# Performance work log

Measured on AMD Instinct MI355X. Metric: run time of the kernel, lower is better.

Reference implementation:

```python
import jax, jax.numpy as jnp
import numpy as np
from jax import lax

D_MODEL = 256; D_HEAD = 32; NHEAD = 8; WIN = 8; TOPK = 8; DMID = 1024
B = 2; H = 128; WD = 128
BN_EPS = 1e-5; ATT_EPS = 1e-6

def _bn(x, g, b, m, v):
    # inference-mode BatchNorm2d over NCHW
    s = g / jnp.sqrt(v + BN_EPS)
    return x * s[None, :, None, None] + (b - m * s)[None, :, None, None]

def _gelu(x):
    return jax.nn.gelu(x, approximate=False)  # torch nn.GELU default (erf)

def _conv1x1(x, w, bias=None):
    y = jnp.einsum('bchw,oc->bohw', x, w)
    if bias is not None:
        y = y + bias[None, :, None, None]
    return y

def _to_win(t):
    b, d, h, wd = t.shape
    nh, nw = h // WIN, wd // WIN
    t = t.reshape(b, d, nh, WIN, nw, WIN).transpose(0, 2, 4, 3, 5, 1)
    return t.reshape(b, nh * nw, WIN * WIN, d)

def _from_win(m, h, wd):
    b, n, w2, d = m.shape
    nh, nw = h // WIN, wd // WIN
    m = m.reshape(b, nh, nw, WIN, WIN, d).transpose(0, 5, 1, 3, 2, 4)
    return m.reshape(b, d, h, wd)

def _linear_attention(q, k, v):
    # LoFTR linear attention. q: [n, L, H, D]; k, v: [n, S, H, D]
    Q = jax.nn.elu(q) + 1.0
    K = jax.nn.elu(k) + 1.0
    s_len = v.shape[1]
    vals = v / s_len
    KV = jnp.einsum('nshd,nshv->nhdv', K, vals)
    Z = 1.0 / (jnp.einsum('nlhd,nhd->nlh', Q, K.sum(axis=1)) + ATT_EPS)
    return jnp.einsum('nlhd,nhdv,nlh->nlhv', Q, KV, Z) * s_len

def _topk_window_attention(q, k, v):
    # partition into WINxWIN windows, select top-K key windows per query window
    # by mean-pooled window similarity, gather them, attend within each window.
    b, d, h, wd = q.shape
    qw, kw, vw = _to_win(q), _to_win(k), _to_win(v)  # [b, N, W2, d]
    n = qw.shape[1]; w2 = WIN * WIN
    sim = jnp.einsum('bnd,bmd->bnm', qw.mean(axis=2), kw.mean(axis=2))
    idx = lax.top_k(sim, TOPK)[1]  # [b, N, K]
    gather = jax.vmap(lambda t, i: t[i])  # over batch: [N,W2,d],[N,K] -> [N,K,W2,d]
    kg = gather(kw, idx).reshape(b, n, TOPK * w2, d)
    vg = gather(vw, idx).reshape(b, n, TOPK * w2, d)
    Q = qw.reshape(b * n, w2, NHEAD, D_HEAD)
    K = kg.reshape(b * n, TOPK * w2, NHEAD, D_HEAD)
    V = vg.reshape(b * n, TOPK * w2, NHEAD, D_HEAD)
    out = _linear_attention(Q, K, V).reshape(b, n, w2, d)
    return _from_win(out, h, wd)

def _forward(x0, bn0_g, bn0_b, bn0_m, bn0_v, q_w, k_w, v_w, merge_w, merge_b,
             mlp_w1, bn1_g, bn1_b, bn1_m, bn1_v, mlp_dw,
             bn2_g, bn2_b, bn2_m, bn2_v, mlp_w2, bn3_g, bn3_b, bn3_m, bn3_v):
    _x = _gelu(_bn(x0, bn0_g, bn0_b, bn0_m, bn0_v))  # pre_normact (x1 = x0)
    q = _conv1x1(_x, q_w); k = _conv1x1(_x, k_w); v = _conv1x1(_x, v_w)
    msg = _topk_window_attention(q, k, v)
    x = x0 + _conv1x1(msg, merge_w, merge_b)  # merge + residual (DropPath=id)
    # MB mlp block: 1x1 -> BN -> GELU -> dw3x3 -> BN -> GELU -> 1x1 -> BN
    y = _conv1x1(x, mlp_w1)
    y = _gelu(_bn(y, bn1_g, bn1_b, bn1_m, bn1_v))
    y = lax.conv_general_dilated(y, mlp_dw, (1, 1), 'SAME',
                                 feature_group_count=DMID,
                                 dimension_numbers=('NCHW', 'OIHW', 'NCHW'))
    y = _gelu(_bn(y, bn2_g, bn2_b, bn2_m, bn2_v))
    y = _conv1x1(y, mlp_w2)
    y = _bn(y, bn3_g, bn3_b, bn3_m, bn3_v)
    return x + y

def setup_inputs() -> dict:
    ks = jax.random.split(jax.random.key(0), 26)
    nrm = lambda i, shape, s=1.0: jax.random.normal(ks[i], shape, jnp.float32) * s
    uni = lambda i, shape: jax.random.uniform(ks[i], shape, jnp.float32, 0.5, 1.5)
    sc = float(1.0 / np.sqrt(D_MODEL))
    return {
        'x0': nrm(0, (B, D_MODEL, H, WD)),
        'bn0_g': uni(1, (D_MODEL,)), 'bn0_b': nrm(2, (D_MODEL,), 0.1),
        'bn0_m': nrm(3, (D_MODEL,), 0.1), 'bn0_v': uni(4, (D_MODEL,)),
        'q_w': nrm(5, (D_MODEL, D_MODEL), sc),
        'k_w': nrm(6, (D_MODEL, D_MODEL), sc),
        'v_w': nrm(7, (D_MODEL, D_MODEL), sc),
        'merge_w': nrm(8, (D_MODEL, D_MODEL), sc), 'merge_b': nrm(9, (D_MODEL,), 0.1),
        'mlp_w1': nrm(10, (DMID, D_MODEL), sc),
        'bn1_g': uni(11, (DMID,)), 'bn1_b': nrm(12, (DMID,), 0.1),
        'bn1_m': nrm(13, (DMID,), 0.1), 'bn1_v': uni(14, (DMID,)),
        'mlp_dw': nrm(15, (DMID, 1, 3, 3), 1.0 / 3.0),
        'bn2_g': uni(16, (DMID,)), 'bn2_b': nrm(17, (DMID,), 0.1),
        'bn2_m': nrm(18, (DMID,), 0.1), 'bn2_v': uni(19, (DMID,)),
        'mlp_w2': nrm(20, (D_MODEL, DMID), float(1.0 / np.sqrt(DMID))),
        'bn3_g': uni(21, (D_MODEL,)), 'bn3_b': nrm(22, (D_MODEL,), 0.1),
        'bn3_m': nrm(23, (D_MODEL,), 0.1), 'bn3_v': uni(24, (D_MODEL,)),
    }

def reference(x0, bn0_g, bn0_b, bn0_m, bn0_v, q_w, k_w, v_w, merge_w, merge_b,
              mlp_w1, bn1_g, bn1_b, bn1_m, bn1_v, mlp_dw,
              bn2_g, bn2_b, bn2_m, bn2_v, mlp_w2, bn3_g, bn3_b, bn3_m, bn3_v):
    return _forward(x0, bn0_g, bn0_b, bn0_m, bn0_v, q_w, k_w, v_w, merge_w, merge_b,
                    mlp_w1, bn1_g, bn1_b, bn1_m, bn1_v, mlp_dw,
                    bn2_g, bn2_b, bn2_m, bn2_v, mlp_w2, bn3_g, bn3_b, bn3_m, bn3_v)
```

## Files before the change

kernel.cpp:

```cpp
#include <hip/hip_runtime.h>
#include <hip/hip_bf16.h>
#include <type_traits>

typedef __hip_bfloat16 bf16;
typedef __attribute__((ext_vector_type(8))) short s16x8;
typedef __attribute__((ext_vector_type(4))) short s16x4;
typedef __attribute__((ext_vector_type(4))) float f32x4;

#define DEVI __device__ __forceinline__

DEVI float bf2f(bf16 x) { return __bfloat162float(x); }
DEVI float to_f(float x) { return x; }
DEVI float to_f(bf16 x) { return __bfloat162float(x); }
DEVI float gelu_f(float x) {
  const float y = x * 0.7071067811865476f;
  const float a = fabsf(y);
  const float t = __builtin_amdgcn_rcpf(1.0f + 0.3275911f * a);
  const float p = t * (0.254829592f + t * (-0.284496736f +
                  t * (1.421413741f + t * (-1.453152027f + t * 1.061405429f))));
  const float e = __expf(-a * a);
  const float erfv = copysignf(1.0f - p * e, y);
  return 0.5f * x * (1.0f + erfv);
}
DEVI float elu1(float x) { return x > 0.f ? x + 1.f : __expf(x); }
DEVI float s2f(short s) {
  unsigned u = ((unsigned)(unsigned short)s) << 16;
  float f; __builtin_memcpy(&f, &u, 4); return f;
}
DEVI short f2s(float x) {
  bf16 h = __float2bfloat16(x);
  short s; __builtin_memcpy(&s, &h, 2); return s;
}

__global__ void detect_kernel(const void* x0, int* dflag) {
  const int t = threadIdx.x;
  const bf16* p = (const bf16*)x0;
  float v = bf2f(p[t * 2]);
  bool ok = (fabsf(v) <= 64.0f);
  unsigned long long m = __ballot(ok);
  if (t == 0) dflag[0] = (m == ~0ull) ? 0 : 1;
}

template <typename TIN>
__global__ __launch_bounds__(256) void bnprep_kernel(
    const int* dflag, int want,
    const TIN* g0, const TIN* b0, const TIN* m0, const TIN* v0,
    const TIN* g1, const TIN* b1, const TIN* m1, const TIN* v1,
    const TIN* g2, const TIN* b2, const TIN* m2, const TIN* v2,
    const TIN* g3, const TIN* b3, const TIN* m3, const TIN* v3,
    const TIN* mb, float* out)
{
  if (dflag[0] != want) return;
  int t = threadIdx.x;
  {
    float s = to_f(g0[t]) / sqrtf(to_f(v0[t]) + 1e-5f);
    out[t] = s; out[256 + t] = to_f(b0[t]) - to_f(m0[t]) * s;
  }
  for (int i = t; i < 1024; i += 256) {
    float s = to_f(g1[i]) / sqrtf(to_f(v1[i]) + 1e-5f);
    out[512 + i] = s; out[1536 + i] = to_f(b1[i]) - to_f(m1[i]) * s;
  }
  for (int i = t; i < 1024; i += 256) {
    float s = to_f(g2[i]) / sqrtf(to_f(v2[i]) + 1e-5f);
    out[2560 + i] = s; out[3584 + i] = to_f(b2[i]) - to_f(m2[i]) * s;
  }
  {
    float s = to_f(g3[t]) / sqrtf(to_f(v3[t]) + 1e-5f);
    out[4608 + t] = s; out[4864 + t] = to_f(b3[t]) - to_f(m3[t]) * s;
    out[5120 + t] = to_f(mb[t]);
  }
}

template <typename TIN>
__global__ __launch_bounds__(256) void wconv_kernel(
    const int* dflag, int want,
    const TIN* qw, const TIN* kw, const TIN* vw, const TIN* mw,
    const TIN* w1, const TIN* w2, const TIN* dw, bf16* dst)
{
  if (dflag[0] != want) return;
  int i = blockIdx.x * 256 + threadIdx.x;
  if (i >= 795648) return;
  const TIN* src; int off;
  if (i < 262144) {
    src = (i < 65536) ? qw : (i < 131072) ? kw : (i < 196608) ? vw : mw;
    off = i & 65535;
  } else if (i < 524288) { src = w1; off = i - 262144; }
  else if (i < 786432) { src = w2; off = i - 524288; }
  else {
    src = dw;
    const int o = i - 786432;
    const int tap = o >> 10, m = o & 1023;
    off = m * 9 + tap;
    if (o >= 9216) return;
  }
  dst[i] = __float2bfloat16(to_f(src[off]));
}

template <typename TIN>
__global__ __launch_bounds__(256) void prenorm_t_kernel(
    const int* dflag, int want, const TIN* __restrict__ x0,
    const float* __restrict__ bn, bf16* __restrict__ xhat_t)
{
  if (dflag[0] != want) return;
  __shared__ float T[128][67];
  const int t = threadIdx.x;
  const int tile = blockIdx.x;
  const int b = tile >> 8;
  const int p0 = (tile & 255) * 64;
  const long xbase = (long)b * 4194304 + p0;
  const int px_off = (t & 7) * 8;
  const int chr = t >> 3;
  const int ch8 = (t & 15) * 8;
  const int pxw = t >> 4;
  #pragma unroll
  for (int pass = 0; pass < 2; ++pass) {
    const int Hc = pass * 128;
    __syncthreads();
    #pragma unroll
    for (int cc = 0; cc < 4; ++cc) {
      const int ch = Hc + chr + 32 * cc;
      const TIN* xp = x0 + (long)ch * 16384 + xbase + px_off;
      float v[8];
      if constexpr (sizeof(TIN) == 2) {
        const s16x8 r = *(const s16x8*)xp;
        #pragma unroll
        for (int j = 0; j < 8; ++j) v[j] = s2f(r[j]);
      } else {
        const float4 a = *(const float4*)xp;
        const float4 c = *(const float4*)(xp + 4);
        v[0] = a.x; v[1] = a.y; v[2] = a.z; v[3] = a.w;
        v[4] = c.x; v[5] = c.y; v[6] = c.z; v[7] = c.w;
      }
      const float s0 = bn[ch], t0 = bn[256 + ch];
      #pragma unroll
      for (int j = 0; j < 8; ++j) v[j] = gelu_f(v[j] * s0 + t0);
      float* Tr = &T[chr + 32 * cc][px_off];
      #pragma unroll
      for (int j = 0; j < 8; ++j) Tr[j] = v[j];
    }
    __syncthreads();
    #pragma unroll
    for (int it = 0; it < 4; ++it) {
      const int px = pxw + 16 * it;
      alignas(16) short o[8];
      #pragma unroll
      for (int j = 0; j < 8; ++j) o[j] = f2s(T[ch8 + j][px]);
      *(uint4*)(xhat_t + (long)(b * 16384 + p0 + px) * 256 + Hc + ch8) =
          *(const uint4*)o;
    }
  }
}

template <int MODE, typename TRES = bf16>
__global__ __launch_bounds__(256) void mfma_gemm(
    const int* dflag, int want,
    const bf16* __restrict__ in, const bf16* __restrict__ w,
    void* __restrict__ out, long obase, const void* __restrict__ resv,
    const float* __restrict__ sv, const float* __restrict__ tv,
    float* __restrict__ aux, int N, int M, int K)
{
  if (want >= 0 && dflag[0] != want) return;
  alignas(16) __shared__ char smem[(MODE <= 2) ? 20480 : 34816];
  bf16* inT = (bf16*)smem;
  bf16* wT  = (bf16*)(smem + 10240);
  const int t = threadIdx.x;
  const int n0 = blockIdx.x * 128, m0 = blockIdx.y * 128;
  const int sr = t >> 1, sk = (t & 1) * 16;
  const int wid = t >> 6, lane = t & 63;
  const int nw = (wid & 1) * 64, mw = (wid >> 1) * 64;
  const int l15 = lane & 15, quad = lane >> 4;
  f32x4 acc[4][4];
  #pragma unroll
  for (int i = 0; i < 4; ++i)
    #pragma unroll
    for (int j = 0; j < 4; ++j) acc[i][j] = 0.f;
  long inRow;
  if (MODE == 4) {
    const int bb4 = n0 >> 14, w0 = (n0 & 16383) >> 6;
    const int win = w0 + (sr >> 6);
    const int rr = (sr >> 3) & 7, cc = sr & 7;
    inRow = ((long)(bb4 * 16384 + ((win >> 4) * 8 + rr) * 128
                    + (win & 15) * 8 + cc)) * K + sk;
  } else {
    inRow = (long)(n0 + sr) * K + sk;
  }
  const long wRow = (long)(m0 + sr) * K + sk;
  for (int k0 = 0; k0 < K; k0 += 32) {
    const uint4 a0 = *(const uint4*)(in + inRow + k0);
    const uint4 a1 = *(const uint4*)(in + inRow + k0 + 8);
    const uint4 b0 = *(const uint4*)(w + wRow + k0);
    const uint4 b1 = *(const uint4*)(w + wRow + k0 + 8);
    __syncthreads();
    *(uint4*)(inT + sr * 40 + sk) = a0;
    *(uint4*)(inT + sr * 40 + sk + 8) = a1;
    *(uint4*)(wT + sr * 40 + sk) = b0;
    *(uint4*)(wT + sr * 40 + sk + 8) = b1;
    __syncthreads();
    s16x8 af[4], bfv[4];
    #pragma unroll
    for (int i = 0; i < 4; ++i)
      af[i] = *(const s16x8*)(inT + (nw + i * 16 + l15) * 40 + quad * 8);
    #pragma unroll
    for (int i = 0; i < 4; ++i)
      bfv[i] = *(const s16x8*)(wT + (mw + i * 16 + l15) * 40 + quad * 8);
    #pragma unroll
    for (int i = 0; i < 4; ++i)
      #pragma unroll
      for (int j = 0; j < 4; ++j)
        acc[i][j] = __builtin_amdgcn_mfma_f32_16x16x32_bf16(af[i], bfv[j], acc[i][j], 0, 0, 0);
  }
  if (MODE <= 2) {
    bf16* ob = (bf16*)out;
    const bool doelu = (MODE == 0) && (m0 < 512);
    #pragma unroll
    for (int i = 0; i < 4; ++i) {
      #pragma unroll
      for (int r = 0; r < 4; ++r) {
        const int n = n0 + nw + i * 16 + quad * 4 + r;
        #pragma unroll
        for (int j = 0; j < 4; ++j) {
          const int m = m0 + mw + j * 16 + l15;
          float vv = acc[i][j][r];
          if (MODE == 0) { if (doelu) vv = elu1(vv); }
          if (MODE == 1) {
            const TRES* res = (const TRES*)resv;
            vv += sv[m] + to_f(res[(long)(n >> 14) * 4194304
                                   + (long)m * 16384 + (n & 16383)]);
          }
          if (MODE == 2) vv = gelu_f(vv * sv[m] + tv[m]);
          ob[(long)n * M + m] = __float2bfloat16(vv);
        }
      }
    }
  } else {
    const int isf = (MODE == 3) ? dflag[0] : 0;
    __syncthreads();
    bf16* T = (bf16*)smem;
    #pragma unroll
    for (int i = 0; i < 4; ++i)
      #pragma unroll
      for (int r = 0; r < 4; ++r) {
        const int n = nw + i * 16 + quad * 4 + r;
        #pragma unroll
        for (int j = 0; j < 4; ++j) {
          const int m = mw + j * 16 + l15;
          float vv = acc[i][j][r];
          if (MODE == 3)
            vv = vv * sv[m0 + m] + tv[m0 + m]
               + bf2f(((const bf16*)resv)[(long)(n0 + n) * 256 + m0 + m]);
          else { if (m0 + m < 256) vv = elu1(vv); }
          T[m * 136 + n] = __float2bfloat16(vv);
        }
      }
    __syncthreads();
    const int mr = t >> 1, half = (t & 1) * 64;
    if (MODE == 4) {
      const int bb4 = n0 >> 14, w0 = (n0 & 16383) >> 6;
      const int gm = m0 + mr;
      bf16* bo = (bf16*)out;
      #pragma unroll
      for (int jj = 0; jj < 8; ++jj) {
        const int C = half + jj * 8;
        const int win = w0 + (C >> 6);
        const int pxc = (C & 63) >> 3;
        *(uint4*)(bo + ((long)(bb4 * 256 + win) << 15) + pxc * 4096 + gm * 8) =
            *(const uint4*)(T + mr * 136 + C);
      }
      if (m0 < 256) {
        float s = 0.f;
        const bf16* Tr = T + mr * 136 + half;
        #pragma unroll
        for (int c8 = 0; c8 < 8; ++c8) {
          const s16x8 v = *(const s16x8*)(Tr + c8 * 8);
          #pragma unroll
          for (int e = 0; e < 8; ++e) s += s2f(v[e]);
        }
        aux[(long)(bb4 * 256 + w0 + (half >> 6)) * 256 + gm] = s;
      }
    } else if (!isf) {
      bf16* bo = (bf16*)out + obase;
      #pragma unroll
      for (int jj = 0; jj < 8; ++jj)
        *(uint4*)(bo + (long)(m0 + mr) * N + n0 + half + jj * 8) =
            *(const uint4*)(T + mr * 136 + half + jj * 8);
    } else {
      float* fo = (float*)out + obase;
      #pragma unroll
      for (int jj = 0; jj < 8; ++jj)
        #pragma unroll
        for (int e = 0; e < 8; ++e)
          fo[(long)(m0 + mr) * N + n0 + half + jj * 8 + e] =
              bf2f(T[mr * 136 + half + jj * 8 + e]);
    }
  }
}

template <typename TIN>
__global__ __launch_bounds__(256) void xmean_kernel(const int* dflag, int want,
                                                    const TIN* __restrict__ x0,
                                                    const float* __restrict__ bn,
                                                    float* __restrict__ xm)
{
  if (dflag[0] != want) return;
  int tid = blockIdx.x * 256 + threadIdx.x;
  int n = tid & 255, c = (tid >> 8) & 255, b = tid >> 16;
  const float s0 = bn[c], t0 = bn[256 + c];
  const long base = (long)b * 4194304 + (long)c * 16384 + ((n >> 4) * 8) * 128 + (n & 15) * 8;
  float s = 0.f;
  #pragma unroll
  for (int r = 0; r < 8; ++r)
    #pragma unroll
    for (int cc = 0; cc < 8; ++cc)
      s += gelu_f(to_f(x0[base + r * 128 + cc]) * s0 + t0);
  xm[tid] = s * 0.015625f;
}

template <typename TIN>
__global__ __launch_bounds__(256) void meanproj_kernel(const int* dflag, int want,
    const TIN* __restrict__ qw, const TIN* __restrict__ kw,
    const float* __restrict__ xm, float* __restrict__ qm, float* __restrict__ km)
{
  if (dflag[0] != want) return;
  int tid = blockIdx.x * 256 + threadIdx.x;
  int nw = tid & 255, o = (tid >> 8) & 255, b = tid >> 16;
  float sq = 0.f, sk = 0.f;
  for (int c = 0; c < 256; ++c) {
    const float x = xm[(b * 256 + c) * 256 + nw];
    sq += to_f(qw[o * 256 + c]) * x;
    sk += to_f(kw[o * 256 + c]) * x;
  }
  qm[(b * 256 + o) * 256 + nw] = sq;
  km[(b * 256 + o) * 256 + nw] = sk;
}

__global__ __launch_bounds__(256) void topk_kernel(const float* __restrict__ qm,
                                                   const float* __restrict__ km,
                                                   int* __restrict__ topki)
{
  const int nq = blockIdx.x, b = blockIdx.y, t = threadIdx.x;
  float sim = 0.f;
  for (int c = 0; c < 256; ++c)
    sim += qm[(b * 256 + c) * 256 + nq] * km[(b * 256 + c) * 256 + t];
  __shared__ float vals[256];
  __shared__ float rv[256];
  __shared__ int ri[256];
  vals[t] = sim;
  __syncthreads();
  for (int j = 0; j < 8; ++j) {
    rv[t] = vals[t]; ri[t] = t;
    __syncthreads();
    for (int off = 128; off > 0; off >>= 1) {
      if (t < off) {
        float v2 = rv[t + off]; int i2 = ri[t + off];
        if (v2 > rv[t] || (v2 == rv[t] && i2 < ri[t])) { rv[t] = v2; ri[t] = i2; }
      }
      __syncthreads();
    }
    const int w = ri[0];
    if (t == 0) topki[(b * 256 + nq) * 8 + j] = w;
    __syncthreads();
    if (t == w) vals[t] = -3.0e38f;
    __syncthreads();
  }
}

__global__ __launch_bounds__(256) void attn_kernel(
    const bf16* __restrict__ qbuf, const bf16* __restrict__ kvT,
    const int* __restrict__ topki, const float* __restrict__ S,
    bf16* __restrict__ msg)
{
  __shared__ bf16 kvB[10240];
  __shared__ float ksum_s[256];
  __shared__ float zs2[512];
  const int n = blockIdx.x, b = blockIdx.y, t = threadIdx.x;
  const long bpix = (long)b * 16384;
  const int lane = t & 63, wid = t >> 6;
  const int l15 = lane & 15, quad = lane >> 4;
  const int h0 = wid * 2;
  f32x4 kvacc[2][2][2];
  #pragma unroll
  for (int a = 0; a < 2; ++a)
    #pragma unroll
    for (int c = 0; c < 2; ++c)
      #pragma unroll
      for (int d = 0; d < 2; ++d) kvacc[a][c][d] = 0.f;
  int wsel[8];
  #pragma unroll
  for (int j = 0; j < 8; ++j) wsel[j] = topki[(b * 256 + n) * 8 + j];

  const long kvTb = (long)b * 8388608;
  #pragma unroll 8
  for (int ck = 0; ck < 16; ++ck) {
    const bf16* base = kvT + kvTb + ((long)wsel[ck >> 1] << 15)
                     + ((ck & 1) * 4 + quad) * 4096;
    #pragma unroll
    for (int hs = 0; hs < 2; ++hs) {
      const int cb = (h0 + hs) * 32;
      const s16x8 a0 = *(const s16x8*)(base + (cb + l15) * 8);
      const s16x8 a1 = *(const s16x8*)(base + (cb + 16 + l15) * 8);
      const s16x8 b0 = *(const s16x8*)(base + (256 + cb + l15) * 8);
      const s16x8 b1 = *(const s16x8*)(base + (256 + cb + 16 + l15) * 8);
      kvacc[hs][0][0] = __builtin_amdgcn_mfma_f32_16x16x32_bf16(a0, b0, kvacc[hs][0][0], 0, 0, 0);
      kvacc[hs][0][1] = __builtin_amdgcn_mfma_f32_16x16x32_bf16(a0, b1, kvacc[hs][0][1], 0, 0, 0);
      kvacc[hs][1][0] = __builtin_amdgcn_mfma_f32_16x16x32_bf16(a1, b0, kvacc[hs][1][0], 0, 0, 0);
      kvacc[hs][1][1] = __builtin_amdgcn_mfma_f32_16x16x32_bf16(a1, b1, kvacc[hs][1][1], 0, 0, 0);
    }
  }

  {
    float ks = 0.f;
    #pragma unroll
    for (int j = 0; j < 8; ++j)
      ks += S[((long)b * 256 + wsel[j]) * 256 + t];
    ksum_s[t] = ks;
  }
  #pragma unroll
  for (int hs = 0; hs < 2; ++hs)
    #pragma unroll
    for (int vt = 0; vt < 2; ++vt) {
      const int row = (h0 + hs) * 32 + vt * 16 + l15;
      #pragma unroll
      for (int dt = 0; dt < 2; ++dt) {
        const f32x4 kv = kvacc[hs][dt][vt];
        uint2 u;
        u.x = (unsigned)(unsigned short)f2s(kv[0])
            | ((unsigned)(unsigned short)f2s(kv[1]) << 16);
        u.y = (unsigned)(unsigned short)f2s(kv[2])
            | ((unsigned)(unsigned short)f2s(kv[3]) << 16);
        *(uint2*)(kvB + row * 40 + dt * 16 + quad * 4) = u;
      }
    }
  __syncthreads();

  const int qh0 = (n >> 4) * 8, qw0 = (n & 15) * 8;
  #pragma unroll
  for (int rep = 0; rep < 2; ++rep) {
    const int idx = t + rep * 256;
    const int l = idx >> 3, hh = idx & 7;
    const long gp = bpix + (qh0 + (l >> 3)) * 128 + qw0 + (l & 7);
    const bf16* qp = qbuf + gp * 256 + hh * 32;
    float dot = 0.f;
    #pragma unroll
    for (int k4 = 0; k4 < 4; ++k4) {
      const s16x8 q8 = *(const s16x8*)(qp + k4 * 8);
      const float4 kA = *(const float4*)(ksum_s + hh * 32 + k4 * 8);
      const float4 kB = *(const float4*)(ksum_s + hh * 32 + k4 * 8 + 4);
      dot += s2f(q8[0]) * kA.x + s2f(q8[1]) * kA.y
           + s2f(q8[2]) * kA.z + s2f(q8[3]) * kA.w
           + s2f(q8[4]) * kB.x + s2f(q8[5]) * kB.y
           + s2f(q8[6]) * kB.z + s2f(q8[7]) * kB.w;
    }
    zs2[hh * 64 + l] = 1.f / (dot + 1e-6f);
  }
  __syncthreads();

  #pragma unroll
  for (int hs = 0; hs < 2; ++hs) {
    const int h = h0 + hs;
    const s16x8 B0 = *(const s16x8*)(kvB + (h * 32 + l15) * 40 + quad * 8);
    const s16x8 B1 = *(const s16x8*)(kvB + (h * 32 + 16 + l15) * 40 + quad * 8);
    #pragma unroll
    for (int i = 0; i < 4; ++i) {
      const int lq = i * 16 + l15;
      const long gpa = bpix + (qh0 + (lq >> 3)) * 128 + qw0 + (lq & 7);
      const s16x8 A = *(const s16x8*)(qbuf + gpa * 256 + h * 32 + quad * 8);
      f32x4 o0 = 0.f, o1 = 0.f;
      o0 = __builtin_amdgcn_mfma_f32_16x16x32_bf16(A, B0, o0, 0, 0, 0);
      o1 = __builtin_amdgcn_mfma_f32_16x16x32_bf16(A, B1, o1, 0, 0, 0);
      const float4 z4 = *(const float4*)(zs2 + h * 64 + i * 16 + quad * 4);
      const float zr[4] = {z4.x, z4.y, z4.z, z4.w};
      #pragma unroll
      for (int r = 0; r < 4; ++r) {
        const int lo = i * 16 + quad * 4 + r;
        const long opix = bpix + (qh0 + (lo >> 3)) * 128 + qw0 + (lo & 7);
        msg[opix * 256 + h * 32 + l15] = __float2bfloat16(o0[r] * zr[r]);
        msg[opix * 256 + h * 32 + 16 + l15] = __float2bfloat16(o1[r] * zr[r]);
      }
    }
  }
}

__global__ __launch_bounds__(256) void dwconv_kernel(const bf16* __restrict__ y1,
                                                     const bf16* __restrict__ wdw,
                                                     const float* __restrict__ s2,
                                                     const float* __restrict__ t2,
                                                     bf16* __restrict__ y2)
{
  const int strip = blockIdx.x;
  const int x0 = (strip & 15) * 8;
  const int yy = strip >> 4;
  const int m0 = threadIdx.x * 4;
  float wv[9][4];
  #pragma unroll
  for (int tap = 0; tap < 9; ++tap) {
    const s16x4 w4 = *(const s16x4*)(wdw + tap * 1024 + m0);
    #pragma unroll
    for (int e = 0; e < 4; ++e) wv[tap][e] = s2f(w4[e]);
  }
  float acc[8][4];
  #pragma unroll
  for (int p = 0; p < 8; ++p)
    #pragma unroll
    for (int e = 0; e < 4; ++e) acc[p][e] = 0.f;
  #pragma unroll
  for (int ky = 0; ky < 3; ++ky) {
    const int row = yy + ky - 1;
    if ((unsigned)row < 128u) {
      const bf16* rp = y1 + (long)row * 131072 + m0;
      #pragma unroll
      for (int cr = 0; cr < 10; ++cr) {
        const int xc = x0 + cr - 1;
        if ((unsigned)xc < 128u) {
          const s16x4 v4 = *(const s16x4*)(rp + (long)xc * 1024);
          float vf[4];
          #pragma unroll
          for (int e = 0; e < 4; ++e) vf[e] = s2f(v4[e]);
          #pragma unroll
          for (int kx = 0; kx < 3; ++kx) {
            const int p = cr - kx;
            if (p >= 0 && p < 8) {
              #pragma unroll
              for (int e = 0; e < 4; ++e)
                acc[p][e] += wv[ky * 3 + kx][e] * vf[e];
            }
          }
        }
      }
    }
  }
  const float4 sv = *(const float4*)(s2 + m0);
  const float4 tv = *(const float4*)(t2 + m0);
  #pragma unroll
  for (int p = 0; p < 8; ++p) {
    s16x4 o;
    o[0] = f2s(gelu_f(acc[p][0] * sv.x + tv.x));
    o[1] = f2s(gelu_f(acc[p][1] * sv.y + tv.y));
    o[2] = f2s(gelu_f(acc[p][2] * sv.z + tv.z));
    o[3] = f2s(gelu_f(acc[p][3] * sv.w + tv.w));
    *(s16x4*)(y2 + (long)(yy * 128 + x0 + p) * 1024 + m0) = o;
  }
}

template <typename TIN>
static void stage_dtype_pre(int want, void* const* d_in, hipStream_t stream,
                            const int* dflag, bf16* wb, float* bnbuf,
                            bf16* xhat_t, float* xmean, float* qm, float* km)
{
  bnprep_kernel<TIN><<<1, 256, 0, stream>>>(dflag, want,
      (const TIN*)d_in[1],  (const TIN*)d_in[2],  (const TIN*)d_in[3],  (const TIN*)d_in[4],
      (const TIN*)d_in[11], (const TIN*)d_in[12], (const TIN*)d_in[13], (const TIN*)d_in[14],
      (const TIN*)d_in[16], (const TIN*)d_in[17], (const TIN*)d_in[18], (const TIN*)d_in[19],
      (const TIN*)d_in[21], (const TIN*)d_in[22], (const TIN*)d_in[23], (const TIN*)d_in[24],
      (const TIN*)d_in[9], bnbuf);
  wconv_kernel<TIN><<<3108, 256, 0, stream>>>(dflag, want,
      (const TIN*)d_in[5], (const TIN*)d_in[6], (const TIN*)d_in[7], (const TIN*)d_in[8],
      (const TIN*)d_in[10], (const TIN*)d_in[20], (const TIN*)d_in[15], wb);
  prenorm_t_kernel<TIN><<<512, 256, 0, stream>>>(dflag, want,
      (const TIN*)d_in[0], bnbuf, xhat_t);
  xmean_kernel<TIN><<<512, 256, 0, stream>>>(dflag, want, (const TIN*)d_in[0], bnbuf, xmean);
  meanproj_kernel<TIN><<<512, 256, 0, stream>>>(dflag, want,
      (const TIN*)d_in[5], (const TIN*)d_in[6], xmean, qm, km);
}

extern "C" void kernel_launch(void* const* d_in, const int* in_sizes, int n_in,
                              void* d_out, int out_size, void* d_ws, size_t ws_size,
                              hipStream_t stream) {
  (void)n_in; (void)out_size; (void)ws_size;
  char* W = (char*)d_ws;
  bf16*  xhat_t = (bf16*)(W);
  bf16*  xres   = (bf16*)(W);
  float* Swin   = (float*)(W + 16777216);
  bf16*  qbuf   = (bf16*)(W + 33554432);
  bf16*  kvT    = (bf16*)(W + 50331648);
  bf16*  msg    = (bf16*)(W + 83886080);
  bf16*  y1     = (bf16*)(W + 33554432);
  bf16*  y2     = (bf16*)(W + 67108864);
  char*  S      = W + 100663296;
  bf16*  wb     = (bf16*)(S);
  bf16*  wmb    = wb + 196608;
  bf16*  w1b    = wb + 262144;
  bf16*  w2b    = wb + 524288;
  bf16*  wdwb   = wb + 786432;
  float* bnbuf  = (float*)(S + 1591296);
  float* xmean  = (float*)(S + 1612800);
  float* qm     = (float*)(S + 2137088);
  float* km     = (float*)(S + 2661376);
  int*   topki  = (int*)(S + 3185664);
  int*   dflag  = (int*)(S + 3202048);

  int known = -1;
  if (in_sizes) {
    if (in_sizes[0] == 16777216) known = 0;
    else if (in_sizes[0] == 33554432) known = 1;
  }

  detect_kernel<<<1, 64, 0, stream>>>(d_in[0], dflag);

  if (known != 1)
    stage_dtype_pre<bf16>(0, d_in, stream, dflag, wb, bnbuf, xhat_t, xmean, qm, km);
  if (known != 0)
    stage_dtype_pre<float>(1, d_in, stream, dflag, wb, bnbuf, xhat_t, xmean, qm, km);

  mfma_gemm<0><<<dim3(256, 2), 256, 0, stream>>>(dflag, -1,
      xhat_t, wb, (void*)qbuf, 0, nullptr, nullptr, nullptr, nullptr, 32768, 256, 256);
  mfma_gemm<4><<<dim3(256, 4), 256, 0, stream>>>(dflag, -1,
      xhat_t, wb + 65536, (void*)kvT, 0, nullptr, nullptr, nullptr, Swin, 32768, 512, 256);

  topk_kernel<<<dim3(256, 2), 256, 0, stream>>>(qm, km, topki);
  attn_kernel<<<dim3(256, 2), 256, 0, stream>>>(qbuf, kvT, topki, Swin, msg);

  if (known != 1)
    mfma_gemm<1, bf16><<<dim3(256, 2), 256, 0, stream>>>(dflag, 0,
        msg, wmb, (void*)xres, 0, d_in[0], bnbuf + 5120, nullptr, nullptr, 32768, 256, 256);
  if (known != 0)
    mfma_gemm<1, float><<<dim3(256, 2), 256, 0, stream>>>(dflag, 1,
        msg, wmb, (void*)xres, 0, d_in[0], bnbuf + 5120, nullptr, nullptr, 32768, 256, 256);

  for (int b = 0; b < 2; ++b) {
    bf16* xres_b = xres + (long)b * 4194304;
    mfma_gemm<2><<<dim3(128, 8), 256, 0, stream>>>(dflag, -1,
        xres_b, w1b, (void*)y1, 0, nullptr, bnbuf + 512, bnbuf + 1536, nullptr, 16384, 1024, 256);
    dwconv_kernel<<<2048, 256, 0, stream>>>(y1, wdwb, bnbuf + 2560, bnbuf + 3584, y2);
    mfma_gemm<3><<<dim3(128, 2), 256, 0, stream>>>(dflag, -1,
        y2, w2b, d_out, (long)b * 4194304, xres_b,
        bnbuf + 4608, bnbuf + 4864, nullptr, 16384, 256, 1024);
  }
}
```

Measured before the change: 453.8 us.

## Prefetch next GEMM K-tile into registers and batch MLP stage across both images

```diff
diff --git a/kernel.cpp b/kernel.cpp
--- a/kernel.cpp
+++ b/kernel.cpp
@@ -185,17 +185,23 @@
     inRow = (long)(n0 + sr) * K + sk;
   }
   const long wRow = (long)(m0 + sr) * K + sk;
+  uint4 a0 = *(const uint4*)(in + inRow);
+  uint4 a1 = *(const uint4*)(in + inRow + 8);
+  uint4 b0 = *(const uint4*)(w + wRow);
+  uint4 b1 = *(const uint4*)(w + wRow + 8);
   for (int k0 = 0; k0 < K; k0 += 32) {
-    const uint4 a0 = *(const uint4*)(in + inRow + k0);
-    const uint4 a1 = *(const uint4*)(in + inRow + k0 + 8);
-    const uint4 b0 = *(const uint4*)(w + wRow + k0);
-    const uint4 b1 = *(const uint4*)(w + wRow + k0 + 8);
     __syncthreads();
     *(uint4*)(inT + sr * 40 + sk) = a0;
     *(uint4*)(inT + sr * 40 + sk + 8) = a1;
     *(uint4*)(wT + sr * 40 + sk) = b0;
     *(uint4*)(wT + sr * 40 + sk + 8) = b1;
     __syncthreads();
+    if (k0 + 32 < K) {
+      a0 = *(const uint4*)(in + inRow + k0 + 32);
+      a1 = *(const uint4*)(in + inRow + k0 + 40);
+      b0 = *(const uint4*)(w + wRow + k0 + 32);
+      b1 = *(const uint4*)(w + wRow + k0 + 40);
+    }
     s16x8 af[4], bfv[4];
     #pragma unroll
     for (int i = 0; i < 4; ++i)
@@ -277,20 +283,23 @@
         }
         aux[(long)(bb4 * 256 + w0 + (half >> 6)) * 256 + gm] = s;
       }
-    } else if (!isf) {
-      bf16* bo = (bf16*)out + obase;
-      #pragma unroll
-      for (int jj = 0; jj < 8; ++jj)
-        *(uint4*)(bo + (long)(m0 + mr) * N + n0 + half + jj * 8) =
-            *(const uint4*)(T + mr * 136 + half + jj * 8);
     } else {
-      float* fo = (float*)out + obase;
-      #pragma unroll
-      for (int jj = 0; jj < 8; ++jj)
+      const int bb3 = n0 >> 14, nloc = n0 & 16383;
+      if (!isf) {
+        bf16* bo = (bf16*)out + obase + (long)bb3 * 4194304;
         #pragma unroll
-        for (int e = 0; e < 8; ++e)
-          fo[(long)(m0 + mr) * N + n0 + half + jj * 8 + e] =
-              bf2f(T[mr * 136 + half + jj * 8 + e]);
+        for (int jj = 0; jj < 8; ++jj)
+          *(uint4*)(bo + (long)(m0 + mr) * 16384 + nloc + half + jj * 8) =
+              *(const uint4*)(T + mr * 136 + half + jj * 8);
+      } else {
+        float* fo = (float*)out + obase + (long)bb3 * 4194304;
+        #pragma unroll
+        for (int jj = 0; jj < 8; ++jj)
+          #pragma unroll
+          for (int e = 0; e < 8; ++e)
+            fo[(long)(m0 + mr) * 16384 + nloc + half + jj * 8 + e] =
+                bf2f(T[mr * 136 + half + jj * 8 + e]);
+      }
     }
   }
 }
@@ -487,9 +496,13 @@
                                                      bf16* __restrict__ y2)
 {
   const int strip = blockIdx.x;
-  const int x0 = (strip & 15) * 8;
-  const int yy = strip >> 4;
+  const int bb = strip >> 11;
+  const int sl = strip & 2047;
+  const int x0 = (sl & 15) * 8;
+  const int yy = sl >> 4;
   const int m0 = threadIdx.x * 4;
+  const bf16* y1b = y1 + (long)bb * 16777216;
+  bf16* y2b = y2 + (long)bb * 16777216;
   float wv[9][4];
   #pragma unroll
   for (int tap = 0; tap < 9; ++tap) {
@@ -506,7 +519,7 @@
   for (int ky = 0; ky < 3; ++ky) {
     const int row = yy + ky - 1;
     if ((unsigned)row < 128u) {
-      const bf16* rp = y1 + (long)row * 131072 + m0;
+      const bf16* rp = y1b + (long)row * 131072 + m0;
       #pragma unroll
       for (int cr = 0; cr < 10; ++cr) {
         const int xc = x0 + cr - 1;
@@ -537,7 +550,7 @@
     o[1] = f2s(gelu_f(acc[p][1] * sv.y + tv.y));
     o[2] = f2s(gelu_f(acc[p][2] * sv.z + tv.z));
     o[3] = f2s(gelu_f(acc[p][3] * sv.w + tv.w));
-    *(s16x4*)(y2 + (long)(yy * 128 + x0 + p) * 1024 + m0) = o;
+    *(s16x4*)(y2b + (long)(yy * 128 + x0 + p) * 1024 + m0) = o;
   }
 }
 
@@ -565,7 +578,7 @@
 extern "C" void kernel_launch(void* const* d_in, const int* in_sizes, int n_in,
                               void* d_out, int out_size, void* d_ws, size_t ws_size,
                               hipStream_t stream) {
-  (void)n_in; (void)out_size; (void)ws_size;
+  (void)n_in; (void)out_size;
   char* W = (char*)d_ws;
   bf16*  xhat_t = (bf16*)(W);
   bf16*  xres   = (bf16*)(W);
@@ -573,8 +586,6 @@
   bf16*  qbuf   = (bf16*)(W + 33554432);
   bf16*  kvT    = (bf16*)(W + 50331648);
   bf16*  msg    = (bf16*)(W + 83886080);
-  bf16*  y1     = (bf16*)(W + 33554432);
-  bf16*  y2     = (bf16*)(W + 67108864);
   char*  S      = W + 100663296;
   bf16*  wb     = (bf16*)(S);
   bf16*  wmb    = wb + 196608;
@@ -587,6 +598,9 @@
   float* km     = (float*)(S + 2661376);
   int*   topki  = (int*)(S + 3185664);
   int*   dflag  = (int*)(S + 3202048);
+  const bool big = (ws_size == 0) || (ws_size >= 171966464ull);
+  bf16*  y1     = (bf16*)(W + 33554432);
+  bf16*  y2     = big ? (bf16*)(W + 104857600) : (bf16*)(W + 67108864);
 
   int known = -1;
   if (in_sizes) {
@@ -616,13 +630,21 @@
     mfma_gemm<1, float><<<dim3(256, 2), 256, 0, stream>>>(dflag, 1,
         msg, wmb, (void*)xres, 0, d_in[0], bnbuf + 5120, nullptr, nullptr, 32768, 256, 256);
 
-  for (int b = 0; b < 2; ++b) {
-    bf16* xres_b = xres + (long)b * 4194304;
-    mfma_gemm<2><<<dim3(128, 8), 256, 0, stream>>>(dflag, -1,
-        xres_b, w1b, (void*)y1, 0, nullptr, bnbuf + 512, bnbuf + 1536, nullptr, 16384, 1024, 256);
-    dwconv_kernel<<<2048, 256, 0, stream>>>(y1, wdwb, bnbuf + 2560, bnbuf + 3584, y2);
-    mfma_gemm<3><<<dim3(128, 2), 256, 0, stream>>>(dflag, -1,
-        y2, w2b, d_out, (long)b * 4194304, xres_b,
-        bnbuf + 4608, bnbuf + 4864, nullptr, 16384, 256, 1024);
-  }
-}
+  if (big) {
+    mfma_gemm<2><<<dim3(256, 8), 256, 0, stream>>>(dflag, -1,
+        xres, w1b, (void*)y1, 0, nullptr, bnbuf + 512, bnbuf + 1536, nullptr, 32768, 1024, 256);
+    dwconv_kernel<<<4096, 256, 0, stream>>>(y1, wdwb, bnbuf + 2560, bnbuf + 3584, y2);
+    mfma_gemm<3><<<dim3(256, 2), 256, 0, stream>>>(dflag, -1,
+        y2, w2b, d_out, 0, xres, bnbuf + 4608, bnbuf + 4864, nullptr, 32768, 256, 1024);
+  } else {
+    for (int b = 0; b < 2; ++b) {
+      bf16* xres_b = xres + (long)b * 4194304;
+      mfma_gemm<2><<<dim3(128, 8), 256, 0, stream>>>(dflag, -1,
+          xres_b, w1b, (void*)y1, 0, nullptr, bnbuf + 512, bnbuf + 1536, nullptr, 16384, 1024, 256);
+      dwconv_kernel<<<2048, 256, 0, stream>>>(y1, wdwb, bnbuf + 2560, bnbuf + 3584, y2);
+      mfma_gemm<3><<<dim3(128, 2), 256, 0, stream>>>(dflag, -1,
+          y2, w2b, d_out, (long)b * 4194304, xres_b,
+          bnbuf + 4608, bnbuf + 4864, nullptr, 16384, 256, 1024);
+    }
+  }
+}
```

Measured after the change: 404.0 us. 1.12x faster.
